# Kernel optimization log

Hardware: AMD Instinct MI355X
Metric: run time of the kernel (lower is better)

## Reference

```python
import jax, jax.numpy as jnp
import numpy as np

B, S, D_IN, D_OUT = 4, 2048, 1024, 1024

def setup_inputs() -> dict:
    key = jax.random.key(0)
    k_x, k_q, k_k, k_v = jax.random.split(key, 4)
    return {
        "x": jax.random.normal(k_x, (B, S, D_IN), dtype=jnp.float32),
        "W_query": jax.random.uniform(k_q, (D_IN, D_OUT), dtype=jnp.float32),
        "W_key": jax.random.uniform(k_k, (D_IN, D_OUT), dtype=jnp.float32),
        "W_value": jax.random.uniform(k_v, (D_IN, D_OUT), dtype=jnp.float32),
    }

def reference(x, W_query, W_key, W_value):
    seq_len = x.shape[1]
    d_out = W_key.shape[-1]
    # fused QKV projection: x @ concat([Wq, Wk, Wv], -1), then split
    qkv = x @ jnp.concatenate([W_query, W_key, W_value], axis=-1)  # [B,S,3*d_out]
    query, key, value = jnp.split(qkv, 3, axis=2)
    # raw scores [B,S,S]; causal mask applied BEFORE scaling (as in source)
    attn_weights = jnp.einsum("bqd,bkd->bqk", query, key)
    causal = jnp.triu(jnp.ones((seq_len, seq_len), dtype=bool), k=1)
    attn_weights = jnp.where(causal[None, :, :], -jnp.inf, attn_weights)
    scaled = attn_weights / jnp.asarray(d_out, x.dtype) ** 0.5
    attn_scores = jax.nn.softmax(scaled, axis=-1)  # dropout p=0 -> identity
    context_vectors = jnp.einsum("bqk,bkd->bqd", attn_scores, value)
    return (context_vectors, attn_scores)
```

## Files before the change

### kernel.cpp

```cpp
#include <hip/hip_runtime.h>
#include <cstdint>
#include <cstddef>


#define S_LEN 2048
#define D_DIM 1024
#define NBATCH 4
#define MEG (1024 * 1024)

typedef __attribute__((ext_vector_type(4))) float floatx4;
typedef __attribute__((ext_vector_type(8))) __bf16 bf16x8;
typedef __attribute__((ext_vector_type(8))) short short8v;

__device__ __forceinline__ unsigned short f2bf(float f) {
  union { float f; unsigned u; } v; v.f = f;
  unsigned r = v.u + 0x7FFF + ((v.u >> 16) & 1);
  return (unsigned short)(r >> 16);
}
__device__ __forceinline__ float bf2f(unsigned short h) {
  union { unsigned u; float f; } v; v.u = ((unsigned)h) << 16; return v.f;
}

__device__ __forceinline__ void async_copy16(const void* g, void* l) {
  __builtin_amdgcn_global_load_lds(
      (const __attribute__((address_space(1))) void*)g,
      (__attribute__((address_space(3))) void*)l, 16, 0, 0);
}


__device__ __forceinline__ void gemm_bt_core(
    const short* __restrict__ A, const short* __restrict__ B,
    int lda, int ldb, int kIters, int blockM, int blockN,
    short (*As)[32], short (*Bs)[32], floatx4 (&acc)[4][4])
{
  const int tid  = threadIdx.x;
  const int lane = tid & 63;
  const int wave = tid >> 6;
  const int wm = (wave >> 1) * 64;
  const int wn = (wave & 1) * 64;
  const int fm = lane & 15;
  const int fk = (lane >> 4) * 8;
  const int r0 = tid >> 2;
  const int c0 = (tid & 3) * 8;

  floatx4 zero = {0.f, 0.f, 0.f, 0.f};
  #pragma unroll
  for (int i = 0; i < 4; ++i)
    #pragma unroll
    for (int j = 0; j < 4; ++j)
      acc[i][j] = zero;

  const short* a0 = A + (size_t)(blockM + r0) * lda + c0;
  const short* a1 = a0 + (size_t)64 * lda;
  const short* b0 = B + (size_t)(blockN + r0) * ldb + c0;
  const short* b1 = b0 + (size_t)64 * ldb;
  short* as0 = &As[r0][c0];
  short* as1 = &As[r0 + 64][c0];
  short* bs0 = &Bs[r0][c0];
  short* bs1 = &Bs[r0 + 64][c0];

  for (int kt = 0; kt < kIters; ++kt) {
    const int kb = kt * 32;
    async_copy16(a0 + kb, as0);
    async_copy16(a1 + kb, as1);
    async_copy16(b0 + kb, bs0);
    async_copy16(b1 + kb, bs1);
    __syncthreads();
    bf16x8 af[4], bfr[4];
    #pragma unroll
    for (int i = 0; i < 4; ++i)
      af[i] = *(const bf16x8*)(&As[wm + i * 16 + fm][fk]);
    #pragma unroll
    for (int j = 0; j < 4; ++j)
      bfr[j] = *(const bf16x8*)(&Bs[wn + j * 16 + fm][fk]);
    #pragma unroll
    for (int i = 0; i < 4; ++i)
      #pragma unroll
      for (int j = 0; j < 4; ++j)
        acc[i][j] = __builtin_amdgcn_mfma_f32_16x16x32_bf16(af[i], bfr[j], acc[i][j], 0, 0, 0);
    __syncthreads();
  }
}

__device__ __forceinline__ void gemm_bt_split_core(
    const short* __restrict__ Ah, const short* __restrict__ Al,
    const short* __restrict__ Bh, const short* __restrict__ Bl,
    int lda, int ldb, int kIters, int blockM, int blockN,
    short (*AsH)[32], short (*AsL)[32], short (*BsH)[32], short (*BsL)[32],
    floatx4 (&acc)[4][4])
{
  const int tid  = threadIdx.x;
  const int lane = tid & 63;
  const int wave = tid >> 6;
  const int wm = (wave >> 1) * 64;
  const int wn = (wave & 1) * 64;
  const int fm = lane & 15;
  const int fk = (lane >> 4) * 8;
  const int r0 = tid >> 2;
  const int c0 = (tid & 3) * 8;

  floatx4 zero = {0.f, 0.f, 0.f, 0.f};
  #pragma unroll
  for (int i = 0; i < 4; ++i)
    #pragma unroll
    for (int j = 0; j < 4; ++j)
      acc[i][j] = zero;

  const size_t oa0 = (size_t)(blockM + r0) * lda + c0;
  const size_t oa1 = oa0 + (size_t)64 * lda;
  const size_t ob0 = (size_t)(blockN + r0) * ldb + c0;
  const size_t ob1 = ob0 + (size_t)64 * ldb;
  short* lah0 = &AsH[r0][c0]; short* lah1 = &AsH[r0 + 64][c0];
  short* lal0 = &AsL[r0][c0]; short* lal1 = &AsL[r0 + 64][c0];
  short* lbh0 = &BsH[r0][c0]; short* lbh1 = &BsH[r0 + 64][c0];
  short* lbl0 = &BsL[r0][c0]; short* lbl1 = &BsL[r0 + 64][c0];

  for (int kt = 0; kt < kIters; ++kt) {
    const int kb = kt * 32;
    async_copy16(Ah + oa0 + kb, lah0);
    async_copy16(Ah + oa1 + kb, lah1);
    async_copy16(Al + oa0 + kb, lal0);
    async_copy16(Al + oa1 + kb, lal1);
    async_copy16(Bh + ob0 + kb, lbh0);
    async_copy16(Bh + ob1 + kb, lbh1);
    async_copy16(Bl + ob0 + kb, lbl0);
    async_copy16(Bl + ob1 + kb, lbl1);
    __syncthreads();
    bf16x8 ah[4], al[4], bh[4], bl[4];
    #pragma unroll
    for (int i = 0; i < 4; ++i) {
      ah[i] = *(const bf16x8*)(&AsH[wm + i * 16 + fm][fk]);
      al[i] = *(const bf16x8*)(&AsL[wm + i * 16 + fm][fk]);
    }
    #pragma unroll
    for (int j = 0; j < 4; ++j) {
      bh[j] = *(const bf16x8*)(&BsH[wn + j * 16 + fm][fk]);
      bl[j] = *(const bf16x8*)(&BsL[wn + j * 16 + fm][fk]);
    }
    #pragma unroll
    for (int i = 0; i < 4; ++i)
      #pragma unroll
      for (int j = 0; j < 4; ++j) {
        acc[i][j] = __builtin_amdgcn_mfma_f32_16x16x32_bf16(ah[i], bh[j], acc[i][j], 0, 0, 0);
        acc[i][j] = __builtin_amdgcn_mfma_f32_16x16x32_bf16(ah[i], bl[j], acc[i][j], 0, 0, 0);
        acc[i][j] = __builtin_amdgcn_mfma_f32_16x16x32_bf16(al[i], bh[j], acc[i][j], 0, 0, 0);
      }
    __syncthreads();
  }
}


__global__ __launch_bounds__(256) void k_cvt_w(
    const float* __restrict__ wq, const float* __restrict__ wk,
    const float* __restrict__ wv,
    short* __restrict__ wqh, short* __restrict__ wql,
    short* __restrict__ wkh, short* __restrict__ wkl,
    short* __restrict__ wvt, float* __restrict__ muSum)
{
  const int bid = blockIdx.x;
  const int tid = threadIdx.x;
  if (bid < 1024) {
    const float4* src;
    short *dh, *dl;
    size_t idx;
    if (bid < 512) {
      idx = (size_t)bid * 256 + tid;
      src = (const float4*)wq; dh = wqh; dl = wql;
    } else {
      idx = (size_t)(bid - 512) * 256 + tid;
      src = (const float4*)wk; dh = wkh; dl = wkl;
    }
    const float4 u4 = src[idx * 2];
    const float4 w4 = src[idx * 2 + 1];
    float f[8] = {u4.x, u4.y, u4.z, u4.w, w4.x, w4.y, w4.z, w4.w};
    short8v oh, ol;
    #pragma unroll
    for (int e = 0; e < 8; ++e) {
      const unsigned short h = f2bf(f[e]);
      oh[e] = (short)h;
      ol[e] = (short)f2bf(f[e] - bf2f(h));
    }
    *(short8v*)(dh + idx * 8) = oh;
    *(short8v*)(dl + idx * 8) = ol;
  } else {
    if (bid == 1024) {
      float4 z = {0.f, 0.f, 0.f, 0.f};
      ((float4*)muSum)[tid] = z;
    }
    const int rem = bid - 1024;
    const int bx = rem & 31, by = rem >> 5;
    const int tx = tid & 31, ty = tid >> 5;
    __shared__ float tile[32][33];
    const int colIn = bx * 32 + tx;
    #pragma unroll
    for (int i = 0; i < 4; ++i) {
      const int rowIn = by * 32 + ty + i * 8;
      tile[ty + i * 8][tx] = wv[(size_t)rowIn * D_DIM + colIn];
    }
    __syncthreads();
    const int colOut = by * 32 + tx;
    #pragma unroll
    for (int i = 0; i < 4; ++i) {
      const int rowOut = bx * 32 + ty + i * 8;
      wvt[(size_t)rowOut * D_DIM + colOut] = (short)f2bf(tile[tx][ty + i * 8]);
    }
  }
}


__global__ __launch_bounds__(256) void k_m_cvtx(
    const short* __restrict__ wqh, const short* __restrict__ wql,
    const short* __restrict__ wkh, const short* __restrict__ wkl,
    short* __restrict__ mth, short* __restrict__ mtl,
    float* __restrict__ muSum,
    const float4* __restrict__ x,
    short* __restrict__ xh, short* __restrict__ xl)
{
  __shared__ alignas(16) short AsH[2][64][32];
  __shared__ alignas(16) short AsL[2][64][32];
  __shared__ alignas(16) short BsH[2][64][32];
  __shared__ alignas(16) short BsL[2][64][32];
  const int g = blockIdx.x;
  const int tid = threadIdx.x;

  if (g < 256) {
    floatx4 acc[2][2];
    const int blockM = (g >> 4) * 64;
    const int blockN = (g & 15) * 64;
    const int lane = tid & 63, wave = tid >> 6;
    const int wm = (wave >> 1) * 32, wn = (wave & 1) * 32;
    const int fm = lane & 15, fk = (lane >> 4) * 8;

    floatx4 zero = {0.f, 0.f, 0.f, 0.f};
    #pragma unroll
    for (int i = 0; i < 2; ++i)
      #pragma unroll
      for (int j = 0; j < 2; ++j)
        acc[i][j] = zero;

    const int sr = tid >> 2;
    const int sc = (tid & 3) * 8;
    const short* ah0 = wkh + (size_t)(blockM + sr) * D_DIM + sc;
    const short* al0 = wkl + (size_t)(blockM + sr) * D_DIM + sc;
    const short* bh0 = wqh + (size_t)(blockN + sr) * D_DIM + sc;
    const short* bl0 = wql + (size_t)(blockN + sr) * D_DIM + sc;
    short* ahB = &AsH[0][0][0]; short* alB = &AsL[0][0][0];
    short* bhB = &BsH[0][0][0]; short* blB = &BsL[0][0][0];
    const int l0 = tid * 8, l1 = (tid + 256) * 8;

    for (int kt = 0; kt < 16; ++kt) {
      const int kb = kt * 64;
      async_copy16(ah0 + kb, ahB + l0);
      async_copy16(ah0 + kb + 32, ahB + l1);
      async_copy16(al0 + kb, alB + l0);
      async_copy16(al0 + kb + 32, alB + l1);
      async_copy16(bh0 + kb, bhB + l0);
      async_copy16(bh0 + kb + 32, bhB + l1);
      async_copy16(bl0 + kb, blB + l0);
      async_copy16(bl0 + kb + 32, blB + l1);
      __syncthreads();
      #pragma unroll
      for (int ks = 0; ks < 2; ++ks) {
        bf16x8 ah[2], al[2], bh[2], bl[2];
        #pragma unroll
        for (int i = 0; i < 2; ++i) {
          ah[i] = *(const bf16x8*)(&AsH[ks][wm + i * 16 + fm][fk]);
          al[i] = *(const bf16x8*)(&AsL[ks][wm + i * 16 + fm][fk]);
        }
        #pragma unroll
        for (int j = 0; j < 2; ++j) {
          bh[j] = *(const bf16x8*)(&BsH[ks][wn + j * 16 + fm][fk]);
          bl[j] = *(const bf16x8*)(&BsL[ks][wn + j * 16 + fm][fk]);
        }
        #pragma unroll
        for (int i = 0; i < 2; ++i)
          #pragma unroll
          for (int j = 0; j < 2; ++j) {
            acc[i][j] = __builtin_amdgcn_mfma_f32_16x16x32_bf16(ah[i], bh[j], acc[i][j], 0, 0, 0);
            acc[i][j] = __builtin_amdgcn_mfma_f32_16x16x32_bf16(ah[i], bl[j], acc[i][j], 0, 0, 0);
            acc[i][j] = __builtin_amdgcn_mfma_f32_16x16x32_bf16(al[i], bh[j], acc[i][j], 0, 0, 0);
          }
      }
      __syncthreads();
    }

    const int rb = wm + ((lane >> 4) << 2);
    const int cb = wn + (lane & 15);
    #pragma unroll
    for (int i = 0; i < 2; ++i)
      #pragma unroll
      for (int j = 0; j < 2; ++j) {
        const int n = blockN + cb + j * 16;
        #pragma unroll
        for (int r = 0; r < 2 * 2; ++r) {
          const int m = blockM + rb + i * 16 + r;
          const float f = acc[i][j][r];
          const unsigned short h = f2bf(f);
          mth[(size_t)m * D_DIM + n] = (short)h;
          mtl[(size_t)m * D_DIM + n] = (short)f2bf(f - bf2f(h));
        }
      }
    #pragma unroll
    for (int i = 0; i < 2; ++i)
      #pragma unroll
      for (int r = 0; r < 4; ++r) {
        float v = acc[i][0][r] + acc[i][1][r];
        v += __shfl_xor(v, 1); v += __shfl_xor(v, 2);
        v += __shfl_xor(v, 4); v += __shfl_xor(v, 8);
        if ((lane & 15) == 0)
          atomicAdd(&muSum[blockM + rb + i * 16 + r], v);
      }
  } else {
    const size_t idx = (size_t)(g - 256) * 256 + tid;
    const float4 u4 = x[idx * 2];
    const float4 w4 = x[idx * 2 + 1];
    float f[8] = {u4.x, u4.y, u4.z, u4.w, w4.x, w4.y, w4.z, w4.w};
    short8v oh, ol;
    #pragma unroll
    for (int e = 0; e < 8; ++e) {
      const unsigned short h = f2bf(f[e]);
      oh[e] = (short)h;
      ol[e] = (short)f2bf(f[e] - bf2f(h));
    }
    *(short8v*)(xh + idx * 8) = oh;
    *(short8v*)(xl + idx * 8) = ol;
  }
}


__global__ __launch_bounds__(256) void k_rowstats(
    const short* __restrict__ xh, const short* __restrict__ xl,
    const float* __restrict__ muSum, float* __restrict__ sq, float* __restrict__ u)
{
  const int r = blockIdx.x, tid = threadIdx.x;
  const ushort4 h = *(const ushort4*)(xh + (size_t)r * D_DIM + tid * 4);
  const ushort4 l = *(const ushort4*)(xl + (size_t)r * D_DIM + tid * 4);
  const float4 m4 = *(const float4*)(muSum + tid * 4);
  const float x0 = bf2f(h.x) + bf2f(l.x);
  const float x1 = bf2f(h.y) + bf2f(l.y);
  const float x2 = bf2f(h.z) + bf2f(l.z);
  const float x3 = bf2f(h.w) + bf2f(l.w);
  float s = x0 + x1 + x2 + x3;
  float uu = m4.x * x0 + m4.y * x1 + m4.z * x2 + m4.w * x3;
  #pragma unroll
  for (int off = 32; off > 0; off >>= 1) {
    s  += __shfl_xor(s, off);
    uu += __shfl_xor(uu, off);
  }
  __shared__ float ps[4], pu[4];
  if ((tid & 63) == 0) { ps[tid >> 6] = s; pu[tid >> 6] = uu; }
  __syncthreads();
  if (tid == 0) {
    sq[r] = ps[0] + ps[1] + ps[2] + ps[3];
    u[r]  = (pu[0] + pu[1] + pu[2] + pu[3]) * (1.0f / 1024.0f);
  }
}


__global__ __launch_bounds__(256) void k_gemm_n(
    const short* __restrict__ xh, const short* __restrict__ xl,
    const short* __restrict__ mth, const short* __restrict__ mtl,
    const float* __restrict__ sq, const float* __restrict__ muSum,
    short* __restrict__ nh, short* __restrict__ nl)
{
  __shared__ alignas(16) short AsH[128][32];
  __shared__ alignas(16) short AsL[128][32];
  __shared__ alignas(16) short BsH[128][32];
  __shared__ alignas(16) short BsL[128][32];
  floatx4 acc[4][4];
  const int blockM = blockIdx.y * 128;
  const int blockN = blockIdx.x * 128;
  gemm_bt_split_core(xh, xl, mth, mtl, D_DIM, D_DIM, D_DIM / 32,
                     blockM, blockN, AsH, AsL, BsH, BsL, acc);

  const int tid = threadIdx.x, lane = tid & 63, wave = tid >> 6;
  const int wm = (wave >> 1) * 64, wn = (wave & 1) * 64;
  const int rb = wm + ((lane >> 4) << 2);
  const int cb = wn + (lane & 15);
  #pragma unroll
  for (int i = 0; i < 4; ++i)
    #pragma unroll
    for (int j = 0; j < 4; ++j) {
      const int n = blockN + cb + j * 16;
      const float muv = muSum[n] * (1.0f / 1024.0f);
      #pragma unroll
      for (int r = 0; r < 4; ++r) {
        const int m = blockM + rb + i * 16 + r;
        const float f = acc[i][j][r] - sq[m] * muv;
        const unsigned short h = f2bf(f);
        nh[(size_t)m * D_DIM + n] = (short)h;
        nl[(size_t)m * D_DIM + n] = (short)f2bf(f - bf2f(h));
      }
    }
}


__global__ __launch_bounds__(256) void k_gemm_sv(
    const short* __restrict__ nh, const short* __restrict__ nl,
    const short* __restrict__ xh, const short* __restrict__ xl,
    const float* __restrict__ sq, const float* __restrict__ u,
    const short* __restrict__ wvt, float* __restrict__ attn,
    short* __restrict__ vt)
{
  __shared__ alignas(16) short AsH[128][32];
  __shared__ alignas(16) short AsL[128][32];
  __shared__ alignas(16) short BsH[128][32];
  __shared__ alignas(16) short BsL[128][32];
  floatx4 acc[4][4];

  const int g = blockIdx.x;
  const int tid = threadIdx.x, lane = tid & 63, wave = tid >> 6;
  const int wm = (wave >> 1) * 64, wn = (wave & 1) * 64;
  const int rb = wm + ((lane >> 4) << 2);
  const int cb = wn + (lane & 15);

  if (g < 544) {
    const int item = (g & 7) * 68 + (g >> 3);
    const int b = item / 136;
    int t = item - b * 136;
    int band = 0;
    while (t >= 58 - 16 * band) { t -= 58 - 16 * band; ++band; }
    int bi = band * 4;
    for (;;) {
      const int w = bi - band * 4 + 1;
      const int ww = w < 4 ? w : 4;
      if (t < ww) break;
      t -= ww; ++bi;
    }
    const int bj = band * 4 + t;

    const size_t boff = (size_t)b * S_LEN * D_DIM;
    gemm_bt_split_core(nh + boff, nl + boff, xh + boff, xl + boff,
                       D_DIM, D_DIM, D_DIM / 32, bi * 128, bj * 128,
                       AsH, AsL, BsH, BsL, acc);

    float* out = attn + (size_t)b * S_LEN * S_LEN;
    const int rowBase = (b << 11) + bi * 128;
    const int colBase = (b << 11) + bj * 128;
    #pragma unroll
    for (int j = 0; j < 4; ++j) {
      const int n = bj * 128 + cb + j * 16;
      const float uv = u[colBase + cb + j * 16];
      #pragma unroll
      for (int i = 0; i < 4; ++i)
        #pragma unroll
        for (int r = 0; r < 4; ++r) {
          const int m = bi * 128 + rb + i * 16 + r;
          const float sv = sq[rowBase + rb + i * 16 + r];
          out[(size_t)m * S_LEN + n] = acc[i][j][r] + sv * uv;
        }
    }
  } else {
    const int vb = g - 544;
    const int blockM = (vb >> 3) * 128;
    const int blockN = (vb & 7) * 128;
    gemm_bt_core(xh, wvt, D_DIM, D_DIM, D_DIM / 32, blockM, blockN,
                 AsH, BsH, acc);
    #pragma unroll
    for (int i = 0; i < 4; ++i)
      #pragma unroll
      for (int j = 0; j < 4; ++j) {
        const int n = blockN + cb + j * 16;
        const int m0 = blockM + rb + i * 16;
        const int b = m0 >> 11;
        const int s0 = m0 & (S_LEN - 1);
        ushort4 pk;
        pk.x = f2bf(acc[i][j][0]); pk.y = f2bf(acc[i][j][1]);
        pk.z = f2bf(acc[i][j][2]); pk.w = f2bf(acc[i][j][3]);
        *(ushort4*)(vt + ((size_t)b * D_DIM + n) * S_LEN + s0) = pk;
      }
  }
}


__global__ __launch_bounds__(256) void k_softmax(float* __restrict__ attn,
                                                 short* __restrict__ pb) {
  const int b = blockIdx.x >> 11;
  const int q = blockIdx.x & (S_LEN - 1);
  float* row  = attn + ((size_t)b * S_LEN + q) * S_LEN;
  short* prow = pb   + ((size_t)b * S_LEN + q) * S_LEN;
  const int tid = threadIdx.x;
  const int k0 = tid * 8;
  const int kBand = ((q >> 7) + 1) << 7;
  __shared__ float sMax[4], sSum[4];

  float v[8];
  if (k0 <= q) {
    const float4 a0 = *(const float4*)(row + k0);
    const float4 a1 = *(const float4*)(row + k0 + 4);
    v[0] = a0.x; v[1] = a0.y; v[2] = a0.z; v[3] = a0.w;
    v[4] = a1.x; v[5] = a1.y; v[6] = a1.z; v[7] = a1.w;
  } else {
    #pragma unroll
    for (int e = 0; e < 8; ++e) v[e] = -3.0e38f;
  }

  float mx = -3.0e38f;
  #pragma unroll
  for (int e = 0; e < 8; ++e) {
    v[e] = (k0 + e <= q) ? v[e] : -3.0e38f;
    mx = fmaxf(mx, v[e]);
  }
  #pragma unroll
  for (int off = 32; off > 0; off >>= 1) mx = fmaxf(mx, __shfl_xor(mx, off));
  if ((tid & 63) == 0) sMax[tid >> 6] = mx;
  __syncthreads();
  mx = fmaxf(fmaxf(sMax[0], sMax[1]), fmaxf(sMax[2], sMax[3]));

  float s = 0.f;
  #pragma unroll
  for (int e = 0; e < 8; ++e) {
    const float p = (k0 + e <= q) ? __expf((v[e] - mx) * 0.03125f) : 0.f;
    v[e] = p;
    s += p;
  }
  #pragma unroll
  for (int off = 32; off > 0; off >>= 1) s += __shfl_xor(s, off);
  if ((tid & 63) == 0) sSum[tid >> 6] = s;
  __syncthreads();
  s = sSum[0] + sSum[1] + sSum[2] + sSum[3];
  const float inv = 1.0f / s;

  float o[8];
  #pragma unroll
  for (int e = 0; e < 8; ++e) o[e] = v[e] * inv;
  float4 w0 = {o[0], o[1], o[2], o[3]};
  float4 w1 = {o[4], o[5], o[6], o[7]};
  *(float4*)(row + k0) = w0;
  *(float4*)(row + k0 + 4) = w1;
  if (k0 < kBand) {
    ushort4 p0, p1;
    p0.x = f2bf(o[0]); p0.y = f2bf(o[1]); p0.z = f2bf(o[2]); p0.w = f2bf(o[3]);
    p1.x = f2bf(o[4]); p1.y = f2bf(o[5]); p1.z = f2bf(o[6]); p1.w = f2bf(o[7]);
    *(ushort4*)(prow + k0) = p0;
    *(ushort4*)(prow + k0 + 4) = p1;
  }
}


__global__ __launch_bounds__(256) void k_gemm_ctx(
    const short* __restrict__ pb, const short* __restrict__ vt,
    float* __restrict__ ctx)
{
  __shared__ alignas(16) short As2[2][128][32];
  __shared__ alignas(16) short Bs2[2][128][32];
  floatx4 acc[4][4];
  const int b = blockIdx.z;
  const int by = 15 - blockIdx.y;
  const int blockM = by * 128;
  const int blockN = blockIdx.x * 128;
  const int kIters = (by + 1) * 2;
  const short* A = pb + (size_t)b * S_LEN * S_LEN;
  const short* B = vt + (size_t)b * D_DIM * S_LEN;

  const int tid = threadIdx.x, lane = tid & 63, wave = tid >> 6;
  const int wm = (wave >> 1) * 64, wn = (wave & 1) * 64;
  const int fm = lane & 15, fk = (lane >> 4) * 8;
  const int r0 = tid >> 2, c0 = (tid & 3) * 8;

  floatx4 zero = {0.f, 0.f, 0.f, 0.f};
  #pragma unroll
  for (int i = 0; i < 4; ++i)
    #pragma unroll
    for (int j = 0; j < 4; ++j)
      acc[i][j] = zero;

  const short* a0 = A + (size_t)(blockM + r0) * S_LEN + c0;
  const short* a1 = a0 + (size_t)64 * S_LEN;
  const short* b0 = B + (size_t)(blockN + r0) * S_LEN + c0;
  const short* b1 = b0 + (size_t)64 * S_LEN;
  short* asBase = &As2[0][0][0];
  short* bsBase = &Bs2[0][0][0];
  short* as0 = asBase + (size_t)tid * 8;
  short* as1 = asBase + (size_t)(tid + 256) * 8;
  short* as2 = asBase + (size_t)(tid + 512) * 8;
  short* as3 = asBase + (size_t)(tid + 768) * 8;
  short* bs0 = bsBase + (size_t)tid * 8;
  short* bs1 = bsBase + (size_t)(tid + 256) * 8;
  short* bs2 = bsBase + (size_t)(tid + 512) * 8;
  short* bs3 = bsBase + (size_t)(tid + 768) * 8;

  for (int kt = 0; kt < kIters; ++kt) {
    const int kb = kt * 64;
    async_copy16(a0 + kb, as0);
    async_copy16(a1 + kb, as1);
    async_copy16(a0 + kb + 32, as2);
    async_copy16(a1 + kb + 32, as3);
    async_copy16(b0 + kb, bs0);
    async_copy16(b1 + kb, bs1);
    async_copy16(b0 + kb + 32, bs2);
    async_copy16(b1 + kb + 32, bs3);
    __syncthreads();
    #pragma unroll
    for (int ks = 0; ks < 2; ++ks) {
      bf16x8 af[4], bfr[4];
      #pragma unroll
      for (int i = 0; i < 4; ++i)
        af[i] = *(const bf16x8*)(&As2[ks][wm + i * 16 + fm][fk]);
      #pragma unroll
      for (int j = 0; j < 4; ++j)
        bfr[j] = *(const bf16x8*)(&Bs2[ks][wn + j * 16 + fm][fk]);
      #pragma unroll
      for (int i = 0; i < 4; ++i)
        #pragma unroll
        for (int j = 0; j < 4; ++j)
          acc[i][j] = __builtin_amdgcn_mfma_f32_16x16x32_bf16(af[i], bfr[j], acc[i][j], 0, 0, 0);
    }
    __syncthreads();
  }

  float* out = ctx + (size_t)b * S_LEN * D_DIM;
  const int rb = wm + ((lane >> 4) << 2);
  const int cb = wn + (lane & 15);
  #pragma unroll
  for (int i = 0; i < 4; ++i)
    #pragma unroll
    for (int j = 0; j < 4; ++j) {
      const int n = blockN + cb + j * 16;
      #pragma unroll
      for (int r = 0; r < 4; ++r) {
        const int m = blockM + rb + i * 16 + r;
        out[(size_t)m * D_DIM + n] = acc[i][j][r];
      }
    }
}


extern "C" void kernel_launch(void* const* d_in, const int* in_sizes, int n_in,
                              void* d_out, int out_size, void* d_ws, size_t ws_size,
                              hipStream_t stream) {
  const float* x  = (const float*)d_in[0];
  const float* wq = (const float*)d_in[1];
  const float* wk = (const float*)d_in[2];
  const float* wv = (const float*)d_in[3];

  float* out  = (float*)d_out;
  float* ctx  = out;
  float* attn = out + (size_t)NBATCH * S_LEN * D_DIM;

  short* ws  = (short*)d_ws;
  short* xh  = ws;
  short* xl  = xh + (size_t)8 * MEG;
  short* wqh = xl + (size_t)8 * MEG;
  short* wql = wqh + (size_t)1 * MEG;
  short* wkh = wql + (size_t)1 * MEG;
  short* wkl = wkh + (size_t)1 * MEG;
  short* wvt = wkl + (size_t)1 * MEG;
  short* mth = wvt + (size_t)1 * MEG;
  short* mtl = mth + (size_t)1 * MEG;
  short* nh  = mtl + (size_t)1 * MEG;
  short* nl  = nh + (size_t)8 * MEG;
  short* vt  = nl + (size_t)8 * MEG;
  short* pb  = nh;
  float* fb  = (float*)(vt + (size_t)8 * MEG);
  float* muS = fb;
  float* sq  = fb + 1024;
  float* u   = sq + 8192;

  k_cvt_w<<<2048, 256, 0, stream>>>(wq, wk, wv, wqh, wql, wkh, wkl, wvt, muS);
  k_m_cvtx<<<4352, 256, 0, stream>>>(wqh, wql, wkh, wkl, mth, mtl, muS,
                                     (const float4*)x, xh, xl);
  k_rowstats<<<8192, 256, 0, stream>>>(xh, xl, muS, sq, u);
  k_gemm_n<<<dim3(8, 64), 256, 0, stream>>>(xh, xl, mth, mtl, sq, muS, nh, nl);
  k_gemm_sv<<<1056, 256, 0, stream>>>(nh, nl, xh, xl, sq, u, wvt, attn, vt);
  k_softmax<<<NBATCH * S_LEN, 256, 0, stream>>>(attn, pb);
  k_gemm_ctx<<<dim3(8, 16, 4), 256, 0, stream>>>(pb, vt, ctx);
}
```

Baseline: 369.8 us.

## Double-buffer LDS tiles in GEMM cores to overlap global loads with MFMA

Converts the shared GEMM cores (plain and hi/lo split) to double-buffered LDS staging. The next k-tile is issued via global_load_lds before computing on the current one, and each iteration ends with a single vmcnt wait plus a raw barrier. The ctx GEMM now reuses the common core with 32-wide k steps instead of its own 64-wide single-buffered loop. This is meant to hide global memory latency behind MFMA work, at the cost of doubled LDS per block, which may lower occupancy.

```diff
diff --git a/kernel.cpp b/kernel.cpp
--- a/kernel.cpp
+++ b/kernel.cpp
@@ -27,11 +27,15 @@
       (__attribute__((address_space(3))) void*)l, 16, 0, 0);
 }
 
+#define VMCNT0() asm volatile("s_waitcnt vmcnt(0)" ::: "memory")
+#define RAW_BAR() __builtin_amdgcn_s_barrier()
+#define SCHED_PIN() __builtin_amdgcn_sched_barrier(0)
+
 
 __device__ __forceinline__ void gemm_bt_core(
     const short* __restrict__ A, const short* __restrict__ B,
     int lda, int ldb, int kIters, int blockM, int blockN,
-    short (*As)[32], short (*Bs)[32], floatx4 (&acc)[4][4])
+    short (*As)[128][32], short (*Bs)[128][32], floatx4 (&acc)[4][4])
 {
   const int tid  = threadIdx.x;
   const int lane = tid & 63;
@@ -54,31 +58,36 @@
   const short* a1 = a0 + (size_t)64 * lda;
   const short* b0 = B + (size_t)(blockN + r0) * ldb + c0;
   const short* b1 = b0 + (size_t)64 * ldb;
-  short* as0 = &As[r0][c0];
-  short* as1 = &As[r0 + 64][c0];
-  short* bs0 = &Bs[r0][c0];
-  short* bs1 = &Bs[r0 + 64][c0];
+
+  auto stage = [&](int bf, int kb) {
+    async_copy16(a0 + kb, &As[bf][r0][c0]);
+    async_copy16(a1 + kb, &As[bf][r0 + 64][c0]);
+    async_copy16(b0 + kb, &Bs[bf][r0][c0]);
+    async_copy16(b1 + kb, &Bs[bf][r0 + 64][c0]);
+  };
+
+  stage(0, 0);
+  VMCNT0();
+  RAW_BAR();
 
   for (int kt = 0; kt < kIters; ++kt) {
-    const int kb = kt * 32;
-    async_copy16(a0 + kb, as0);
-    async_copy16(a1 + kb, as1);
-    async_copy16(b0 + kb, bs0);
-    async_copy16(b1 + kb, bs1);
-    __syncthreads();
+    const int cur = kt & 1;
+    if (kt + 1 < kIters) stage(cur ^ 1, (kt + 1) * 32);
     bf16x8 af[4], bfr[4];
     #pragma unroll
     for (int i = 0; i < 4; ++i)
-      af[i] = *(const bf16x8*)(&As[wm + i * 16 + fm][fk]);
+      af[i] = *(const bf16x8*)(&As[cur][wm + i * 16 + fm][fk]);
     #pragma unroll
     for (int j = 0; j < 4; ++j)
-      bfr[j] = *(const bf16x8*)(&Bs[wn + j * 16 + fm][fk]);
+      bfr[j] = *(const bf16x8*)(&Bs[cur][wn + j * 16 + fm][fk]);
     #pragma unroll
     for (int i = 0; i < 4; ++i)
       #pragma unroll
       for (int j = 0; j < 4; ++j)
         acc[i][j] = __builtin_amdgcn_mfma_f32_16x16x32_bf16(af[i], bfr[j], acc[i][j], 0, 0, 0);
-    __syncthreads();
+    SCHED_PIN();
+    VMCNT0();
+    RAW_BAR();
   }
 }
 
@@ -86,7 +95,8 @@
     const short* __restrict__ Ah, const short* __restrict__ Al,
     const short* __restrict__ Bh, const short* __restrict__ Bl,
     int lda, int ldb, int kIters, int blockM, int blockN,
-    short (*AsH)[32], short (*AsL)[32], short (*BsH)[32], short (*BsL)[32],
+    short (*AsH)[128][32], short (*AsL)[128][32],
+    short (*BsH)[128][32], short (*BsL)[128][32],
     floatx4 (&acc)[4][4])
 {
   const int tid  = threadIdx.x;
@@ -110,32 +120,35 @@
   const size_t oa1 = oa0 + (size_t)64 * lda;
   const size_t ob0 = (size_t)(blockN + r0) * ldb + c0;
   const size_t ob1 = ob0 + (size_t)64 * ldb;
-  short* lah0 = &AsH[r0][c0]; short* lah1 = &AsH[r0 + 64][c0];
-  short* lal0 = &AsL[r0][c0]; short* lal1 = &AsL[r0 + 64][c0];
-  short* lbh0 = &BsH[r0][c0]; short* lbh1 = &BsH[r0 + 64][c0];
-  short* lbl0 = &BsL[r0][c0]; short* lbl1 = &BsL[r0 + 64][c0];
+
+  auto stage = [&](int bf, int kb) {
+    async_copy16(Ah + oa0 + kb, &AsH[bf][r0][c0]);
+    async_copy16(Ah + oa1 + kb, &AsH[bf][r0 + 64][c0]);
+    async_copy16(Al + oa0 + kb, &AsL[bf][r0][c0]);
+    async_copy16(Al + oa1 + kb, &AsL[bf][r0 + 64][c0]);
+    async_copy16(Bh + ob0 + kb, &BsH[bf][r0][c0]);
+    async_copy16(Bh + ob1 + kb, &BsH[bf][r0 + 64][c0]);
+    async_copy16(Bl + ob0 + kb, &BsL[bf][r0][c0]);
+    async_copy16(Bl + ob1 + kb, &BsL[bf][r0 + 64][c0]);
+  };
+
+  stage(0, 0);
+  VMCNT0();
+  RAW_BAR();
 
   for (int kt = 0; kt < kIters; ++kt) {
-    const int kb = kt * 32;
-    async_copy16(Ah + oa0 + kb, lah0);
-    async_copy16(Ah + oa1 + kb, lah1);
-    async_copy16(Al + oa0 + kb, lal0);
-    async_copy16(Al + oa1 + kb, lal1);
-    async_copy16(Bh + ob0 + kb, lbh0);
-    async_copy16(Bh + ob1 + kb, lbh1);
-    async_copy16(Bl + ob0 + kb, lbl0);
-    async_copy16(Bl + ob1 + kb, lbl1);
-    __syncthreads();
+    const int cur = kt & 1;
+    if (kt + 1 < kIters) stage(cur ^ 1, (kt + 1) * 32);
     bf16x8 ah[4], al[4], bh[4], bl[4];
     #pragma unroll
     for (int i = 0; i < 4; ++i) {
-      ah[i] = *(const bf16x8*)(&AsH[wm + i * 16 + fm][fk]);
-      al[i] = *(const bf16x8*)(&AsL[wm + i * 16 + fm][fk]);
+      ah[i] = *(const bf16x8*)(&AsH[cur][wm + i * 16 + fm][fk]);
+      al[i] = *(const bf16x8*)(&AsL[cur][wm + i * 16 + fm][fk]);
     }
     #pragma unroll
     for (int j = 0; j < 4; ++j) {
-      bh[j] = *(const bf16x8*)(&BsH[wn + j * 16 + fm][fk]);
-      bl[j] = *(const bf16x8*)(&BsL[wn + j * 16 + fm][fk]);
+      bh[j] = *(const bf16x8*)(&BsH[cur][wn + j * 16 + fm][fk]);
+      bl[j] = *(const bf16x8*)(&BsL[cur][wn + j * 16 + fm][fk]);
     }
     #pragma unroll
     for (int i = 0; i < 4; ++i)
@@ -145,7 +158,9 @@
         acc[i][j] = __builtin_amdgcn_mfma_f32_16x16x32_bf16(ah[i], bl[j], acc[i][j], 0, 0, 0);
         acc[i][j] = __builtin_amdgcn_mfma_f32_16x16x32_bf16(al[i], bh[j], acc[i][j], 0, 0, 0);
       }
-    __syncthreads();
+    SCHED_PIN();
+    VMCNT0();
+    RAW_BAR();
   }
 }
 
@@ -363,10 +378,10 @@
     const float* __restrict__ sq, const float* __restrict__ muSum,
     short* __restrict__ nh, short* __restrict__ nl)
 {
-  __shared__ alignas(16) short AsH[128][32];
-  __shared__ alignas(16) short AsL[128][32];
-  __shared__ alignas(16) short BsH[128][32];
-  __shared__ alignas(16) short BsL[128][32];
+  __shared__ alignas(16) short AsH[2][128][32];
+  __shared__ alignas(16) short AsL[2][128][32];
+  __shared__ alignas(16) short BsH[2][128][32];
+  __shared__ alignas(16) short BsL[2][128][32];
   floatx4 acc[4][4];
   const int blockM = blockIdx.y * 128;
   const int blockN = blockIdx.x * 128;
@@ -402,10 +417,10 @@
     const short* __restrict__ wvt, float* __restrict__ attn,
     short* __restrict__ vt)
 {
-  __shared__ alignas(16) short AsH[128][32];
-  __shared__ alignas(16) short AsL[128][32];
-  __shared__ alignas(16) short BsH[128][32];
-  __shared__ alignas(16) short BsL[128][32];
+  __shared__ alignas(16) short AsH[2][128][32];
+  __shared__ alignas(16) short AsL[2][128][32];
+  __shared__ alignas(16) short BsH[2][128][32];
+  __shared__ alignas(16) short BsL[2][128][32];
   floatx4 acc[4][4];
 
   const int g = blockIdx.x;
@@ -549,67 +564,15 @@
   const int by = 15 - blockIdx.y;
   const int blockM = by * 128;
   const int blockN = blockIdx.x * 128;
-  const int kIters = (by + 1) * 2;
+  const int kIters = (by + 1) * 4;
   const short* A = pb + (size_t)b * S_LEN * S_LEN;
   const short* B = vt + (size_t)b * D_DIM * S_LEN;
 
+  gemm_bt_core(A, B, S_LEN, S_LEN, kIters, blockM, blockN, As2, Bs2, acc);
+
+  float* out = ctx + (size_t)b * S_LEN * D_DIM;
   const int tid = threadIdx.x, lane = tid & 63, wave = tid >> 6;
   const int wm = (wave >> 1) * 64, wn = (wave & 1) * 64;
-  const int fm = lane & 15, fk = (lane >> 4) * 8;
-  const int r0 = tid >> 2, c0 = (tid & 3) * 8;
-
-  floatx4 zero = {0.f, 0.f, 0.f, 0.f};
-  #pragma unroll
-  for (int i = 0; i < 4; ++i)
-    #pragma unroll
-    for (int j = 0; j < 4; ++j)
-      acc[i][j] = zero;
-
-  const short* a0 = A + (size_t)(blockM + r0) * S_LEN + c0;
-  const short* a1 = a0 + (size_t)64 * S_LEN;
-  const short* b0 = B + (size_t)(blockN + r0) * S_LEN + c0;
-  const short* b1 = b0 + (size_t)64 * S_LEN;
-  short* asBase = &As2[0][0][0];
-  short* bsBase = &Bs2[0][0][0];
-  short* as0 = asBase + (size_t)tid * 8;
-  short* as1 = asBase + (size_t)(tid + 256) * 8;
-  short* as2 = asBase + (size_t)(tid + 512) * 8;
-  short* as3 = asBase + (size_t)(tid + 768) * 8;
-  short* bs0 = bsBase + (size_t)tid * 8;
-  short* bs1 = bsBase + (size_t)(tid + 256) * 8;
-  short* bs2 = bsBase + (size_t)(tid + 512) * 8;
-  short* bs3 = bsBase + (size_t)(tid + 768) * 8;
-
-  for (int kt = 0; kt < kIters; ++kt) {
-    const int kb = kt * 64;
-    async_copy16(a0 + kb, as0);
-    async_copy16(a1 + kb, as1);
-    async_copy16(a0 + kb + 32, as2);
-    async_copy16(a1 + kb + 32, as3);
-    async_copy16(b0 + kb, bs0);
-    async_copy16(b1 + kb, bs1);
-    async_copy16(b0 + kb + 32, bs2);
-    async_copy16(b1 + kb + 32, bs3);
-    __syncthreads();
-    #pragma unroll
-    for (int ks = 0; ks < 2; ++ks) {
-      bf16x8 af[4], bfr[4];
-      #pragma unroll
-      for (int i = 0; i < 4; ++i)
-        af[i] = *(const bf16x8*)(&As2[ks][wm + i * 16 + fm][fk]);
-      #pragma unroll
-      for (int j = 0; j < 4; ++j)
-        bfr[j] = *(const bf16x8*)(&Bs2[ks][wn + j * 16 + fm][fk]);
-      #pragma unroll
-      for (int i = 0; i < 4; ++i)
-        #pragma unroll
-        for (int j = 0; j < 4; ++j)
-          acc[i][j] = __builtin_amdgcn_mfma_f32_16x16x32_bf16(af[i], bfr[j], acc[i][j], 0, 0, 0);
-    }
-    __syncthreads();
-  }
-
-  float* out = ctx + (size_t)b * S_LEN * D_DIM;
   const int rb = wm + ((lane >> 4) << 2);
   const int cb = wn + (lane & 15);
   #pragma unroll
```

After: 393.2 us. 1.06x slower.

## Double-buffer split-bf16 GEMMs with 8-wave 256x128 tiles and swizzled LDS

Applied to the files above, without the earlier changes.

Replaces the single-buffered 128x128 GEMM cores used by the N and score/V projection kernels with 512-thread cores computing 256x128 tiles. The cores double-buffer LDS, prefetching the next K slice in two halves interleaved with MFMA phases, and raise wave priority during MFMA. LDS columns are XOR-swizzled to avoid bank conflicts, and the grids are remapped: causal block enumeration now walks 256-row bands. The aim is to hide global-load latency and double operand reuse, at the cost of more LDS per block (lower occupancy), and it leans on raw barriers plus vmcnt waits being placed correctly.

```diff
diff --git a/kernel.cpp b/kernel.cpp
--- a/kernel.cpp
+++ b/kernel.cpp
@@ -27,66 +27,17 @@
       (__attribute__((address_space(3))) void*)l, 16, 0, 0);
 }
 
-
-__device__ __forceinline__ void gemm_bt_core(
-    const short* __restrict__ A, const short* __restrict__ B,
-    int lda, int ldb, int kIters, int blockM, int blockN,
-    short (*As)[32], short (*Bs)[32], floatx4 (&acc)[4][4])
-{
-  const int tid  = threadIdx.x;
-  const int lane = tid & 63;
-  const int wave = tid >> 6;
-  const int wm = (wave >> 1) * 64;
-  const int wn = (wave & 1) * 64;
-  const int fm = lane & 15;
-  const int fk = (lane >> 4) * 8;
-  const int r0 = tid >> 2;
-  const int c0 = (tid & 3) * 8;
-
-  floatx4 zero = {0.f, 0.f, 0.f, 0.f};
-  #pragma unroll
-  for (int i = 0; i < 4; ++i)
-    #pragma unroll
-    for (int j = 0; j < 4; ++j)
-      acc[i][j] = zero;
-
-  const short* a0 = A + (size_t)(blockM + r0) * lda + c0;
-  const short* a1 = a0 + (size_t)64 * lda;
-  const short* b0 = B + (size_t)(blockN + r0) * ldb + c0;
-  const short* b1 = b0 + (size_t)64 * ldb;
-  short* as0 = &As[r0][c0];
-  short* as1 = &As[r0 + 64][c0];
-  short* bs0 = &Bs[r0][c0];
-  short* bs1 = &Bs[r0 + 64][c0];
-
-  for (int kt = 0; kt < kIters; ++kt) {
-    const int kb = kt * 32;
-    async_copy16(a0 + kb, as0);
-    async_copy16(a1 + kb, as1);
-    async_copy16(b0 + kb, bs0);
-    async_copy16(b1 + kb, bs1);
-    __syncthreads();
-    bf16x8 af[4], bfr[4];
-    #pragma unroll
-    for (int i = 0; i < 4; ++i)
-      af[i] = *(const bf16x8*)(&As[wm + i * 16 + fm][fk]);
-    #pragma unroll
-    for (int j = 0; j < 4; ++j)
-      bfr[j] = *(const bf16x8*)(&Bs[wn + j * 16 + fm][fk]);
-    #pragma unroll
-    for (int i = 0; i < 4; ++i)
-      #pragma unroll
-      for (int j = 0; j < 4; ++j)
-        acc[i][j] = __builtin_amdgcn_mfma_f32_16x16x32_bf16(af[i], bfr[j], acc[i][j], 0, 0, 0);
-    __syncthreads();
-  }
-}
-
-__device__ __forceinline__ void gemm_bt_split_core(
+#define VMCNT0() asm volatile("s_waitcnt vmcnt(0)" ::: "memory")
+#define RAW_BAR() __builtin_amdgcn_s_barrier()
+#define MFMA_BF16 __builtin_amdgcn_mfma_f32_16x16x32_bf16
+
+
+__device__ __forceinline__ void split_core8(
     const short* __restrict__ Ah, const short* __restrict__ Al,
     const short* __restrict__ Bh, const short* __restrict__ Bl,
     int lda, int ldb, int kIters, int blockM, int blockN,
-    short (*AsH)[32], short (*AsL)[32], short (*BsH)[32], short (*BsL)[32],
+    short (*AsH)[256][32], short (*AsL)[256][32],
+    short (*BsH)[128][32], short (*BsL)[128][32],
     floatx4 (&acc)[4][4])
 {
   const int tid  = threadIdx.x;
@@ -95,9 +46,16 @@
   const int wm = (wave >> 1) * 64;
   const int wn = (wave & 1) * 64;
   const int fm = lane & 15;
-  const int fk = (lane >> 4) * 8;
-  const int r0 = tid >> 2;
-  const int c0 = (tid & 3) * 8;
+  const int fu = lane >> 4;
+
+  int rA[4], sA[4], rB[4], sB[4];
+  #pragma unroll
+  for (int i = 0; i < 4; ++i) {
+    rA[i] = wm + i * 16 + fm;
+    sA[i] = (fu ^ ((rA[i] >> 1) & 3)) * 8;
+    rB[i] = wn + i * 16 + fm;
+    sB[i] = (fu ^ ((rB[i] >> 1) & 3)) * 8;
+  }
 
   floatx4 zero = {0.f, 0.f, 0.f, 0.f};
   #pragma unroll
@@ -106,46 +64,165 @@
     for (int j = 0; j < 4; ++j)
       acc[i][j] = zero;
 
-  const size_t oa0 = (size_t)(blockM + r0) * lda + c0;
-  const size_t oa1 = oa0 + (size_t)64 * lda;
-  const size_t ob0 = (size_t)(blockN + r0) * ldb + c0;
-  const size_t ob1 = ob0 + (size_t)64 * ldb;
-  short* lah0 = &AsH[r0][c0]; short* lah1 = &AsH[r0 + 64][c0];
-  short* lal0 = &AsL[r0][c0]; short* lal1 = &AsL[r0 + 64][c0];
-  short* lbh0 = &BsH[r0][c0]; short* lbh1 = &BsH[r0 + 64][c0];
-  short* lbl0 = &BsL[r0][c0]; short* lbl1 = &BsL[r0 + 64][c0];
+  const int r0 = tid >> 2;
+  const int u0 = tid & 3;
+  const int su = (u0 ^ ((r0 >> 1) & 3)) * 8;
+  const size_t a0 = (size_t)(blockM + r0) * lda + su;
+  const size_t a1 = a0 + (size_t)128 * lda;
+  const size_t b0 = (size_t)(blockN + r0) * ldb + su;
+
+  auto stage0 = [&](int bf, int kb) {
+    async_copy16(Ah + a0 + kb, &AsH[bf][r0][u0 * 8]);
+    async_copy16(Al + a0 + kb, &AsL[bf][r0][u0 * 8]);
+    async_copy16(Bh + b0 + kb, &BsH[bf][r0][u0 * 8]);
+  };
+  auto stage1 = [&](int bf, int kb) {
+    async_copy16(Ah + a1 + kb, &AsH[bf][r0 + 128][u0 * 8]);
+    async_copy16(Al + a1 + kb, &AsL[bf][r0 + 128][u0 * 8]);
+    async_copy16(Bl + b0 + kb, &BsL[bf][r0][u0 * 8]);
+  };
+
+  stage0(0, 0);
+  stage1(0, 0);
+  VMCNT0();
+  RAW_BAR();
 
   for (int kt = 0; kt < kIters; ++kt) {
-    const int kb = kt * 32;
-    async_copy16(Ah + oa0 + kb, lah0);
-    async_copy16(Ah + oa1 + kb, lah1);
-    async_copy16(Al + oa0 + kb, lal0);
-    async_copy16(Al + oa1 + kb, lal1);
-    async_copy16(Bh + ob0 + kb, lbh0);
-    async_copy16(Bh + ob1 + kb, lbh1);
-    async_copy16(Bl + ob0 + kb, lbl0);
-    async_copy16(Bl + ob1 + kb, lbl1);
-    __syncthreads();
-    bf16x8 ah[4], al[4], bh[4], bl[4];
-    #pragma unroll
-    for (int i = 0; i < 4; ++i) {
-      ah[i] = *(const bf16x8*)(&AsH[wm + i * 16 + fm][fk]);
-      al[i] = *(const bf16x8*)(&AsL[wm + i * 16 + fm][fk]);
-    }
+    const int cur = kt & 1;
+    const int kb = (kt + 1) * 32;
+    const bool pf = (kt + 1) < kIters;
+
+    bf16x8 bh[4], bl[4];
     #pragma unroll
     for (int j = 0; j < 4; ++j) {
-      bh[j] = *(const bf16x8*)(&BsH[wn + j * 16 + fm][fk]);
-      bl[j] = *(const bf16x8*)(&BsL[wn + j * 16 + fm][fk]);
-    }
-    #pragma unroll
-    for (int i = 0; i < 4; ++i)
-      #pragma unroll
-      for (int j = 0; j < 4; ++j) {
-        acc[i][j] = __builtin_amdgcn_mfma_f32_16x16x32_bf16(ah[i], bh[j], acc[i][j], 0, 0, 0);
-        acc[i][j] = __builtin_amdgcn_mfma_f32_16x16x32_bf16(ah[i], bl[j], acc[i][j], 0, 0, 0);
-        acc[i][j] = __builtin_amdgcn_mfma_f32_16x16x32_bf16(al[i], bh[j], acc[i][j], 0, 0, 0);
-      }
-    __syncthreads();
+      bh[j] = *(const bf16x8*)(&BsH[cur][rB[j]][sB[j]]);
+      bl[j] = *(const bf16x8*)(&BsL[cur][rB[j]][sB[j]]);
+    }
+    bf16x8 ah0 = *(const bf16x8*)(&AsH[cur][rA[0]][sA[0]]);
+    bf16x8 al0 = *(const bf16x8*)(&AsL[cur][rA[0]][sA[0]]);
+    bf16x8 ah1 = *(const bf16x8*)(&AsH[cur][rA[1]][sA[1]]);
+    bf16x8 al1 = *(const bf16x8*)(&AsL[cur][rA[1]][sA[1]]);
+    if (pf) stage0(cur ^ 1, kb);
+    RAW_BAR();
+    __builtin_amdgcn_s_setprio(1);
+    #pragma unroll
+    for (int j = 0; j < 4; ++j) {
+      acc[0][j] = MFMA_BF16(ah0, bh[j], acc[0][j], 0, 0, 0);
+      acc[0][j] = MFMA_BF16(ah0, bl[j], acc[0][j], 0, 0, 0);
+      acc[0][j] = MFMA_BF16(al0, bh[j], acc[0][j], 0, 0, 0);
+      acc[1][j] = MFMA_BF16(ah1, bh[j], acc[1][j], 0, 0, 0);
+      acc[1][j] = MFMA_BF16(ah1, bl[j], acc[1][j], 0, 0, 0);
+      acc[1][j] = MFMA_BF16(al1, bh[j], acc[1][j], 0, 0, 0);
+    }
+    __builtin_amdgcn_s_setprio(0);
+    RAW_BAR();
+
+    bf16x8 ah2 = *(const bf16x8*)(&AsH[cur][rA[2]][sA[2]]);
+    bf16x8 al2 = *(const bf16x8*)(&AsL[cur][rA[2]][sA[2]]);
+    bf16x8 ah3 = *(const bf16x8*)(&AsH[cur][rA[3]][sA[3]]);
+    bf16x8 al3 = *(const bf16x8*)(&AsL[cur][rA[3]][sA[3]]);
+    if (pf) stage1(cur ^ 1, kb);
+    RAW_BAR();
+    __builtin_amdgcn_s_setprio(1);
+    #pragma unroll
+    for (int j = 0; j < 4; ++j) {
+      acc[2][j] = MFMA_BF16(ah2, bh[j], acc[2][j], 0, 0, 0);
+      acc[2][j] = MFMA_BF16(ah2, bl[j], acc[2][j], 0, 0, 0);
+      acc[2][j] = MFMA_BF16(al2, bh[j], acc[2][j], 0, 0, 0);
+      acc[3][j] = MFMA_BF16(ah3, bh[j], acc[3][j], 0, 0, 0);
+      acc[3][j] = MFMA_BF16(ah3, bl[j], acc[3][j], 0, 0, 0);
+      acc[3][j] = MFMA_BF16(al3, bh[j], acc[3][j], 0, 0, 0);
+    }
+    __builtin_amdgcn_s_setprio(0);
+    VMCNT0();
+    RAW_BAR();
+  }
+}
+
+__device__ __forceinline__ void single_core8(
+    const short* __restrict__ A, const short* __restrict__ B,
+    int lda, int ldb, int kIters, int blockM, int blockN,
+    short (*As)[256][32], short (*Bs)[128][32], floatx4 (&acc)[4][4])
+{
+  const int tid  = threadIdx.x;
+  const int lane = tid & 63;
+  const int wave = tid >> 6;
+  const int wm = (wave >> 1) * 64;
+  const int wn = (wave & 1) * 64;
+  const int fm = lane & 15;
+  const int fu = lane >> 4;
+
+  int rA[4], sA[4], rB[4], sB[4];
+  #pragma unroll
+  for (int i = 0; i < 4; ++i) {
+    rA[i] = wm + i * 16 + fm;
+    sA[i] = (fu ^ ((rA[i] >> 1) & 3)) * 8;
+    rB[i] = wn + i * 16 + fm;
+    sB[i] = (fu ^ ((rB[i] >> 1) & 3)) * 8;
+  }
+
+  floatx4 zero = {0.f, 0.f, 0.f, 0.f};
+  #pragma unroll
+  for (int i = 0; i < 4; ++i)
+    #pragma unroll
+    for (int j = 0; j < 4; ++j)
+      acc[i][j] = zero;
+
+  const int r0 = tid >> 2;
+  const int u0 = tid & 3;
+  const int su = (u0 ^ ((r0 >> 1) & 3)) * 8;
+  const size_t a0 = (size_t)(blockM + r0) * lda + su;
+  const size_t a1 = a0 + (size_t)128 * lda;
+  const size_t b0 = (size_t)(blockN + r0) * ldb + su;
+
+  auto stage0 = [&](int bf, int kb) {
+    async_copy16(A + a0 + kb, &As[bf][r0][u0 * 8]);
+    async_copy16(B + b0 + kb, &Bs[bf][r0][u0 * 8]);
+  };
+  auto stage1 = [&](int bf, int kb) {
+    async_copy16(A + a1 + kb, &As[bf][r0 + 128][u0 * 8]);
+  };
+
+  stage0(0, 0);
+  stage1(0, 0);
+  VMCNT0();
+  RAW_BAR();
+
+  for (int kt = 0; kt < kIters; ++kt) {
+    const int cur = kt & 1;
+    const int kb = (kt + 1) * 32;
+    const bool pf = (kt + 1) < kIters;
+
+    bf16x8 bfr[4];
+    #pragma unroll
+    for (int j = 0; j < 4; ++j)
+      bfr[j] = *(const bf16x8*)(&Bs[cur][rB[j]][sB[j]]);
+    bf16x8 a0f = *(const bf16x8*)(&As[cur][rA[0]][sA[0]]);
+    bf16x8 a1f = *(const bf16x8*)(&As[cur][rA[1]][sA[1]]);
+    if (pf) stage0(cur ^ 1, kb);
+    RAW_BAR();
+    __builtin_amdgcn_s_setprio(1);
+    #pragma unroll
+    for (int j = 0; j < 4; ++j) {
+      acc[0][j] = MFMA_BF16(a0f, bfr[j], acc[0][j], 0, 0, 0);
+      acc[1][j] = MFMA_BF16(a1f, bfr[j], acc[1][j], 0, 0, 0);
+    }
+    __builtin_amdgcn_s_setprio(0);
+    RAW_BAR();
+
+    bf16x8 a2f = *(const bf16x8*)(&As[cur][rA[2]][sA[2]]);
+    bf16x8 a3f = *(const bf16x8*)(&As[cur][rA[3]][sA[3]]);
+    if (pf) stage1(cur ^ 1, kb);
+    RAW_BAR();
+    __builtin_amdgcn_s_setprio(1);
+    #pragma unroll
+    for (int j = 0; j < 4; ++j) {
+      acc[2][j] = MFMA_BF16(a2f, bfr[j], acc[2][j], 0, 0, 0);
+      acc[3][j] = MFMA_BF16(a3f, bfr[j], acc[3][j], 0, 0, 0);
+    }
+    __builtin_amdgcn_s_setprio(0);
+    VMCNT0();
+    RAW_BAR();
   }
 }
 
@@ -276,9 +353,9 @@
         for (int i = 0; i < 2; ++i)
           #pragma unroll
           for (int j = 0; j < 2; ++j) {
-            acc[i][j] = __builtin_amdgcn_mfma_f32_16x16x32_bf16(ah[i], bh[j], acc[i][j], 0, 0, 0);
-            acc[i][j] = __builtin_amdgcn_mfma_f32_16x16x32_bf16(ah[i], bl[j], acc[i][j], 0, 0, 0);
-            acc[i][j] = __builtin_amdgcn_mfma_f32_16x16x32_bf16(al[i], bh[j], acc[i][j], 0, 0, 0);
+            acc[i][j] = MFMA_BF16(ah[i], bh[j], acc[i][j], 0, 0, 0);
+            acc[i][j] = MFMA_BF16(ah[i], bl[j], acc[i][j], 0, 0, 0);
+            acc[i][j] = MFMA_BF16(al[i], bh[j], acc[i][j], 0, 0, 0);
           }
       }
       __syncthreads();
@@ -357,21 +434,23 @@
 }
 
 
-__global__ __launch_bounds__(256) void k_gemm_n(
+__global__ __launch_bounds__(512) void k_gemm_n8(
     const short* __restrict__ xh, const short* __restrict__ xl,
     const short* __restrict__ mth, const short* __restrict__ mtl,
     const float* __restrict__ sq, const float* __restrict__ muSum,
     short* __restrict__ nh, short* __restrict__ nl)
 {
-  __shared__ alignas(16) short AsH[128][32];
-  __shared__ alignas(16) short AsL[128][32];
-  __shared__ alignas(16) short BsH[128][32];
-  __shared__ alignas(16) short BsL[128][32];
+  __shared__ alignas(16) short AsH[2][256][32];
+  __shared__ alignas(16) short AsL[2][256][32];
+  __shared__ alignas(16) short BsH[2][128][32];
+  __shared__ alignas(16) short BsL[2][128][32];
   floatx4 acc[4][4];
-  const int blockM = blockIdx.y * 128;
-  const int blockN = blockIdx.x * 128;
-  gemm_bt_split_core(xh, xl, mth, mtl, D_DIM, D_DIM, D_DIM / 32,
-                     blockM, blockN, AsH, AsL, BsH, BsL, acc);
+  const int g = blockIdx.x;
+  const int swz = (g & 7) * 32 + (g >> 3);
+  const int blockM = (swz >> 3) * 256;
+  const int blockN = (swz & 7) * 128;
+  split_core8(xh, xl, mth, mtl, D_DIM, D_DIM, D_DIM / 32,
+              blockM, blockN, AsH, AsL, BsH, BsL, acc);
 
   const int tid = threadIdx.x, lane = tid & 63, wave = tid >> 6;
   const int wm = (wave >> 1) * 64, wn = (wave & 1) * 64;
@@ -395,17 +474,17 @@
 }
 
 
-__global__ __launch_bounds__(256) void k_gemm_sv(
+__global__ __launch_bounds__(512) void k_gemm_sv8(
     const short* __restrict__ nh, const short* __restrict__ nl,
     const short* __restrict__ xh, const short* __restrict__ xl,
     const float* __restrict__ sq, const float* __restrict__ u,
     const short* __restrict__ wvt, float* __restrict__ attn,
     short* __restrict__ vt)
 {
-  __shared__ alignas(16) short AsH[128][32];
-  __shared__ alignas(16) short AsL[128][32];
-  __shared__ alignas(16) short BsH[128][32];
-  __shared__ alignas(16) short BsL[128][32];
+  __shared__ alignas(16) short AsH[2][256][32];
+  __shared__ alignas(16) short AsL[2][256][32];
+  __shared__ alignas(16) short BsH[2][128][32];
+  __shared__ alignas(16) short BsL[2][128][32];
   floatx4 acc[4][4];
 
   const int g = blockIdx.x;
@@ -414,28 +493,21 @@
   const int rb = wm + ((lane >> 4) << 2);
   const int cb = wn + (lane & 15);
 
-  if (g < 544) {
-    const int item = (g & 7) * 68 + (g >> 3);
-    const int b = item / 136;
-    int t = item - b * 136;
-    int band = 0;
-    while (t >= 58 - 16 * band) { t -= 58 - 16 * band; ++band; }
-    int bi = band * 4;
-    for (;;) {
-      const int w = bi - band * 4 + 1;
-      const int ww = w < 4 ? w : 4;
-      if (t < ww) break;
-      t -= ww; ++bi;
-    }
-    const int bj = band * 4 + t;
+  if (g < 288) {
+    const int item = (g & 7) * 36 + (g >> 3);
+    const int b = item / 72;
+    int t = item - b * 72;
+    int bi = 0;
+    while (t >= 2 * bi + 2) { t -= 2 * bi + 2; ++bi; }
+    const int bj = t;
 
     const size_t boff = (size_t)b * S_LEN * D_DIM;
-    gemm_bt_split_core(nh + boff, nl + boff, xh + boff, xl + boff,
-                       D_DIM, D_DIM, D_DIM / 32, bi * 128, bj * 128,
-                       AsH, AsL, BsH, BsL, acc);
+    split_core8(nh + boff, nl + boff, xh + boff, xl + boff,
+                D_DIM, D_DIM, D_DIM / 32, bi * 256, bj * 128,
+                AsH, AsL, BsH, BsL, acc);
 
     float* out = attn + (size_t)b * S_LEN * S_LEN;
-    const int rowBase = (b << 11) + bi * 128;
+    const int rowBase = (b << 11) + bi * 256;
     const int colBase = (b << 11) + bj * 128;
     #pragma unroll
     for (int j = 0; j < 4; ++j) {
@@ -445,16 +517,16 @@
       for (int i = 0; i < 4; ++i)
         #pragma unroll
         for (int r = 0; r < 4; ++r) {
-          const int m = bi * 128 + rb + i * 16 + r;
+          const int m = bi * 256 + rb + i * 16 + r;
           const float sv = sq[rowBase + rb + i * 16 + r];
           out[(size_t)m * S_LEN + n] = acc[i][j][r] + sv * uv;
         }
     }
   } else {
-    const int vb = g - 544;
-    const int blockM = (vb >> 3) * 128;
+    const int vb = g - 288;
+    const int blockM = (vb >> 3) * 256;
     const int blockN = (vb & 7) * 128;
-    gemm_bt_core(xh, wvt, D_DIM, D_DIM, D_DIM / 32, blockM, blockN,
+    single_core8(xh, wvt, D_DIM, D_DIM, D_DIM / 32, blockM, blockN,
                  AsH, BsH, acc);
     #pragma unroll
     for (int i = 0; i < 4; ++i)
@@ -604,7 +676,7 @@
       for (int i = 0; i < 4; ++i)
         #pragma unroll
         for (int j = 0; j < 4; ++j)
-          acc[i][j] = __builtin_amdgcn_mfma_f32_16x16x32_bf16(af[i], bfr[j], acc[i][j], 0, 0, 0);
+          acc[i][j] = MFMA_BF16(af[i], bfr[j], acc[i][j], 0, 0, 0);
     }
     __syncthreads();
   }
@@ -661,8 +733,8 @@
   k_m_cvtx<<<4352, 256, 0, stream>>>(wqh, wql, wkh, wkl, mth, mtl, muS,
                                      (const float4*)x, xh, xl);
   k_rowstats<<<8192, 256, 0, stream>>>(xh, xl, muS, sq, u);
-  k_gemm_n<<<dim3(8, 64), 256, 0, stream>>>(xh, xl, mth, mtl, sq, muS, nh, nl);
-  k_gemm_sv<<<1056, 256, 0, stream>>>(nh, nl, xh, xl, sq, u, wvt, attn, vt);
+  k_gemm_n8<<<256, 512, 0, stream>>>(xh, xl, mth, mtl, sq, muS, nh, nl);
+  k_gemm_sv8<<<544, 512, 0, stream>>>(nh, nl, xh, xl, sq, u, wvt, attn, vt);
   k_softmax<<<NBATCH * S_LEN, 256, 0, stream>>>(attn, pb);
   k_gemm_ctx<<<dim3(8, 16, 4), 256, 0, stream>>>(pb, vt, ctx);
 }
```

Result: no change. 366.2 us (-1.0%).
